# Optimization experiments

Hardware: AMD Instinct MI355X
Metric: run time of the kernel (lower is better)

## Reference

```python
import jax, jax.numpy as jnp
import numpy as np

B, C, H, W = 16, 64, 256, 256
STRIDE = 2
IN_KS = 3
OUT_KS = 3  # must be odd
HP, WP = H // STRIDE, W // STRIDE


def setup_inputs() -> dict:
    key = jax.random.key(0)
    k1, k2, k3 = jax.random.split(key, 3)
    f = jax.random.normal(k1, (B, C, HP, WP), dtype=jnp.float32)
    # Provenance: for pooled cell (i, j), the argmax location within the
    # IN_KS x IN_KS window anchored at (i*STRIDE, j*STRIDE), as a flat h*w index.
    dy = jax.random.randint(k2, (B, C, HP, WP), 0, IN_KS)
    dx = jax.random.randint(k3, (B, C, HP, WP), 0, IN_KS)
    rows = jnp.clip(jnp.arange(HP)[None, None, :, None] * STRIDE + dy, 0, H - 1)
    cols = jnp.clip(jnp.arange(WP)[None, None, None, :] * STRIDE + dx, 0, W - 1)
    provenance = (rows * W + cols).astype(jnp.int32)
    return {"f": f, "provenance": provenance, "h": H, "w": W}


def reference(f, provenance, h, w):
    b, c, hp, wp = f.shape
    # --- unpool: scatter pooled values to provenance locations in an h*w canvas ---
    vals = f.reshape(b * c, hp * wp)
    idx = provenance.reshape(b * c, hp * wp)
    scatter = lambda i, v: jnp.zeros((h * w,), f.dtype).at[i].set(v)
    up = jax.vmap(scatter)(idx, vals).reshape(b, c, h, w)
    # --- dilation: OUT_KS x OUT_KS windowed max, stride 1, 'same' padding ---
    p = (OUT_KS - 1) // 2
    out = jax.lax.reduce_window(
        up, -jnp.inf, jax.lax.max,
        window_dimensions=(1, 1, OUT_KS, OUT_KS),
        window_strides=(1, 1, 1, 1),
        padding=[(0, 0), (0, 0), (p, p), (p, p)],
    )
    return out
```

## Files before the change

### kernel.cpp

```cpp
#include <hip/hip_runtime.h>
#include <math.h>

#define BATCH 16
#define CHAN  64
#define Hh    256
#define Ww    256
#define HP    128
#define WP    128
#define TH    32
#define TW    32
#define CH    (TH + 2)
#define CW    (TW + 2)
#define CSU   35

typedef unsigned long long u64;

__global__ __launch_bounds__(256) void unpool_dilate_kernel(
    const float* __restrict__ f, const int* __restrict__ prov,
    float* __restrict__ out)
{
    __shared__ u64 s_cell[CH * CSU];

    const int tid = threadIdx.x;
    const int bc  = blockIdx.y;
    const int ty  = blockIdx.x >> 3;
    const int tx  = blockIdx.x & 7;
    const int y0  = ty * TH;
    const int x0  = tx * TW;

    const bool interior = (y0 != 0) & (y0 != Hh - TH) & (x0 != 0) & (x0 != Ww - TW);
    if (interior) {
        #pragma unroll
        for (int it = 0; it < 5; ++it) {
            const int idx = tid + it * 256;
            if (idx < CH * CSU) s_cell[idx] = 0ULL;
        }
    } else {
        #pragma unroll
        for (int it = 0; it < 5; ++it) {
            const int idx = tid + it * 256;
            if (idx < CH * CSU) {
                const int lr = idx / CSU;
                const int lc = idx - lr * CSU;
                const int r  = y0 - 1 + lr;
                const int c  = x0 - 1 + lc;
                const bool in = ((unsigned)r < Hh) & ((unsigned)c < Ww);
                s_cell[idx] = in ? 0ULL : 0xFF800000ULL;
            }
        }
    }

    const int pi_min = (y0 == 0) ? 0 : (y0 / 2 - 1);
    const int pj_min = (x0 == 0) ? 0 : (x0 / 2 - 1);
    const int pi_max = min(HP - 1, y0 / 2 + 16);
    const int pj_max = min(WP - 1, x0 / 2 + 16);
    const size_t in_base = (size_t)bc * (HP * WP);

    __syncthreads();

    #pragma unroll
    for (int it = 0; it < 2; ++it) {
        const int k = tid + it * 256;
        if (k < 18 * 18) {
            const int ki = k / 18;
            const int kj = k - ki * 18;
            const int pi = pi_min + ki;
            const int pj = pj_min + kj;
            if (pi <= pi_max && pj <= pj_max) {
                const int q = pi * WP + pj;
                const int p = prov[in_base + q];
                const int lr = (p >> 8) - y0 + 1;
                const int lc = (p & 255) - x0 + 1;
                if ((unsigned)lr < CH && (unsigned)lc < CW) {
                    const float fv = f[in_base + q];
                    const u64 v = ((u64)(unsigned)(q + 1) << 32) | __float_as_uint(fv);
                    atomicMax(&s_cell[lr * CSU + lc], v);
                }
            }
        }
    }
    __syncthreads();

    const int orow = tid >> 3;
    const int oc0  = (tid & 7) * 4;
    float vm[6];
    #pragma unroll
    for (int j = 0; j < 6; ++j) vm[j] = -INFINITY;
    #pragma unroll
    for (int dr = 0; dr < 3; ++dr) {
        const u64* row = &s_cell[(orow + dr) * CSU + oc0];
        #pragma unroll
        for (int j = 0; j < 6; ++j)
            vm[j] = fmaxf(vm[j], __uint_as_float((unsigned)row[j]));
    }
    float4 res;
    res.x = fmaxf(fmaxf(vm[0], vm[1]), vm[2]);
    res.y = fmaxf(fmaxf(vm[1], vm[2]), vm[3]);
    res.z = fmaxf(fmaxf(vm[2], vm[3]), vm[4]);
    res.w = fmaxf(fmaxf(vm[3], vm[4]), vm[5]);

    const size_t obase = (size_t)bc * (Hh * Ww)
                       + (size_t)(y0 + orow) * Ww + (x0 + oc0);
    *(float4*)(out + obase) = res;
}

extern "C" void kernel_launch(void* const* d_in, const int* in_sizes, int n_in,
                              void* d_out, int out_size, void* d_ws, size_t ws_size,
                              hipStream_t stream) {
    const float* f    = (const float*)d_in[0];
    const int*   prov = (const int*)d_in[1];
    float* out = (float*)d_out;

    dim3 grid((Hh / TH) * (Ww / TW), BATCH * CHAN);
    unpool_dilate_kernel<<<grid, 256, 0, stream>>>(f, prov, out);
}
```

Baseline: 436.5 us.

## Enlarge tiles to 64x64, use 32-bit key atomics and 4x4 register-blocked max

Doubles the tile to 64x64 so that halo and pooled-input overhead per output shrinks. It replaces the 64-bit packed atomicMax with a 32-bit atomicMax on the source index, followed by a resolve pass in which the winning thread writes its float value. Each thread now computes a 4x4 output block, reusing horizontal row maxima across rows to cut shared-memory reads. In exchange it adds an extra barrier and pass, and the -inf border writes are not ordered against other waves' zero-fill stores, which could race.

```diff
diff --git a/kernel.cpp b/kernel.cpp
--- a/kernel.cpp
+++ b/kernel.cpp
@@ -7,63 +7,60 @@
 #define Ww    256
 #define HP    128
 #define WP    128
-#define TH    32
-#define TW    32
-#define CH    (TH + 2)
-#define CW    (TW + 2)
-#define CSU   35
+#define TH    64
+#define TW    64
+#define CH    66
+#define CW    66
+#define CS    68
 
-typedef unsigned long long u64;
+typedef unsigned int u32;
 
-__global__ __launch_bounds__(256) void unpool_dilate_kernel(
+__global__ __launch_bounds__(256, 8) void unpool_dilate_kernel(
     const float* __restrict__ f, const int* __restrict__ prov,
     float* __restrict__ out)
 {
-    __shared__ u64 s_cell[CH * CSU];
+    __shared__ __align__(16) u32 s[CH * CS];
 
     const int tid = threadIdx.x;
     const int bc  = blockIdx.y;
-    const int ty  = blockIdx.x >> 3;
-    const int tx  = blockIdx.x & 7;
+    const int ty  = blockIdx.x >> 2;
+    const int tx  = blockIdx.x & 3;
     const int y0  = ty * TH;
     const int x0  = tx * TW;
 
-    const bool interior = (y0 != 0) & (y0 != Hh - TH) & (x0 != 0) & (x0 != Ww - TW);
-    if (interior) {
+    {
+        uint4* p4 = (uint4*)s;
+        const uint4 z = make_uint4(0u, 0u, 0u, 0u);
         #pragma unroll
         for (int it = 0; it < 5; ++it) {
             const int idx = tid + it * 256;
-            if (idx < CH * CSU) s_cell[idx] = 0ULL;
-        }
-    } else {
-        #pragma unroll
-        for (int it = 0; it < 5; ++it) {
-            const int idx = tid + it * 256;
-            if (idx < CH * CSU) {
-                const int lr = idx / CSU;
-                const int lc = idx - lr * CSU;
-                const int r  = y0 - 1 + lr;
-                const int c  = x0 - 1 + lc;
-                const bool in = ((unsigned)r < Hh) & ((unsigned)c < Ww);
-                s_cell[idx] = in ? 0ULL : 0xFF800000ULL;
-            }
+            if (idx < (CH * CS) / 4) p4[idx] = z;
         }
     }
+    const u32 NEGINF = 0xFF800000u;
+    if (ty == 0 && tid < CW) s[tid] = NEGINF;
+    if (ty == 3 && tid < CW) s[(CH - 1) * CS + tid] = NEGINF;
+    if (tx == 0 && tid < CH) s[tid * CS] = NEGINF;
+    if (tx == 3 && tid < CH) s[tid * CS + (CW - 1)] = NEGINF;
 
-    const int pi_min = (y0 == 0) ? 0 : (y0 / 2 - 1);
-    const int pj_min = (x0 == 0) ? 0 : (x0 / 2 - 1);
-    const int pi_max = min(HP - 1, y0 / 2 + 16);
-    const int pj_max = min(WP - 1, x0 / 2 + 16);
+    const int pi_min = (ty == 0) ? 0 : (ty * 32 - 1);
+    const int pj_min = (tx == 0) ? 0 : (tx * 32 - 1);
+    const int pi_max = min(HP - 1, ty * 32 + 32);
+    const int pj_max = min(WP - 1, tx * 32 + 32);
     const size_t in_base = (size_t)bc * (HP * WP);
 
     __syncthreads();
 
+    int   m_li[5];
+    u32   m_key[5];
+    float m_f[5];
     #pragma unroll
-    for (int it = 0; it < 2; ++it) {
+    for (int it = 0; it < 5; ++it) {
+        m_li[it] = -1;
         const int k = tid + it * 256;
-        if (k < 18 * 18) {
-            const int ki = k / 18;
-            const int kj = k - ki * 18;
+        if (k < 34 * 34) {
+            const int ki = k / 34;
+            const int kj = k - ki * 34;
             const int pi = pi_min + ki;
             const int pj = pj_min + kj;
             if (pi <= pi_max && pj <= pj_max) {
@@ -72,36 +69,54 @@
                 const int lr = (p >> 8) - y0 + 1;
                 const int lc = (p & 255) - x0 + 1;
                 if ((unsigned)lr < CH && (unsigned)lc < CW) {
-                    const float fv = f[in_base + q];
-                    const u64 v = ((u64)(unsigned)(q + 1) << 32) | __float_as_uint(fv);
-                    atomicMax(&s_cell[lr * CSU + lc], v);
+                    const int li = lr * CS + lc;
+                    m_li[it]  = li;
+                    m_key[it] = (u32)(q + 1);
+                    m_f[it]   = f[in_base + q];
+                    atomicMax(&s[li], (u32)(q + 1));
                 }
             }
         }
     }
     __syncthreads();
 
-    const int orow = tid >> 3;
-    const int oc0  = (tid & 7) * 4;
-    float vm[6];
     #pragma unroll
-    for (int j = 0; j < 6; ++j) vm[j] = -INFINITY;
+    for (int it = 0; it < 5; ++it) {
+        if (m_li[it] >= 0 && s[m_li[it]] == m_key[it])
+            s[m_li[it]] = __float_as_uint(m_f[it]);
+    }
+    __syncthreads();
+
+    const float* sf = (const float*)s;
+    const int tr = tid >> 4;
+    const int tc = tid & 15;
+    const int r0 = 4 * tr;
+    const int c0 = 4 * tc;
+
+    float h0[4], h1[4], h2[4];
+    const size_t obase = (size_t)bc * (Hh * Ww) + (size_t)(y0 + r0) * Ww + (x0 + c0);
+
     #pragma unroll
-    for (int dr = 0; dr < 3; ++dr) {
-        const u64* row = &s_cell[(orow + dr) * CSU + oc0];
+    for (int r = 0; r < 6; ++r) {
+        const float* row = sf + (r0 + r) * CS + c0;
+        const float4 a = *(const float4*)row;
+        const float2 b = *(const float2*)(row + 4);
+        float h[4];
+        h[0] = fmaxf(fmaxf(a.x, a.y), a.z);
+        h[1] = fmaxf(fmaxf(a.y, a.z), a.w);
+        h[2] = fmaxf(fmaxf(a.z, a.w), b.x);
+        h[3] = fmaxf(fmaxf(a.w, b.x), b.y);
+        if (r >= 2) {
+            float4 res;
+            res.x = fmaxf(fmaxf(h0[0], h1[0]), h[0]);
+            res.y = fmaxf(fmaxf(h0[1], h1[1]), h[1]);
+            res.z = fmaxf(fmaxf(h0[2], h1[2]), h[2]);
+            res.w = fmaxf(fmaxf(h0[3], h1[3]), h[3]);
+            *(float4*)(out + obase + (size_t)(r - 2) * Ww) = res;
+        }
         #pragma unroll
-        for (int j = 0; j < 6; ++j)
-            vm[j] = fmaxf(vm[j], __uint_as_float((unsigned)row[j]));
+        for (int j = 0; j < 4; ++j) { h0[j] = h1[j]; h1[j] = h[j]; }
     }
-    float4 res;
-    res.x = fmaxf(fmaxf(vm[0], vm[1]), vm[2]);
-    res.y = fmaxf(fmaxf(vm[1], vm[2]), vm[3]);
-    res.z = fmaxf(fmaxf(vm[2], vm[3]), vm[4]);
-    res.w = fmaxf(fmaxf(vm[3], vm[4]), vm[5]);
-
-    const size_t obase = (size_t)bc * (Hh * Ww)
-                       + (size_t)(y0 + orow) * Ww + (x0 + oc0);
-    *(float4*)(out + obase) = res;
 }
 
 extern "C" void kernel_launch(void* const* d_in, const int* in_sizes, int n_in,
```

Result: faster. 376.7 us (-13.7%).

## Replace shared-memory atomic scatter with register gather over 4x4 output patches

Applied to the files above, without the earlier changes.

Drops the shared-memory canvas built with 64-bit atomicMax and replaces it with a gather. Each block stages a 34x34 patch of (provenance, value) pairs in shared memory. Each thread then rebuilds a 6x6 window of the unpooled canvas in registers by comparing relative provenance offsets, and computes a 4x4 output patch. Tiles grow from 32x32 to 64x64, output uses nontemporal vector stores, and launch bounds request 4 blocks per CU. The goal is to remove atomic contention, the canvas initialization pass and extra synchronisation, at the cost of more register pressure and compare/select work per thread.

```diff
diff --git a/kernel.cpp b/kernel.cpp
--- a/kernel.cpp
+++ b/kernel.cpp
@@ -7,101 +7,114 @@
 #define Ww    256
 #define HP    128
 #define WP    128
-#define TH    32
-#define TW    32
-#define CH    (TH + 2)
-#define CW    (TW + 2)
-#define CSU   35
+#define TH    64
+#define TW    64
+#define PR    34
 
-typedef unsigned long long u64;
+typedef float vfloat4 __attribute__((ext_vector_type(4)));
 
-__global__ __launch_bounds__(256) void unpool_dilate_kernel(
+__global__ __launch_bounds__(256, 4) void unpool_dilate_kernel(
     const float* __restrict__ f, const int* __restrict__ prov,
     float* __restrict__ out)
 {
-    __shared__ u64 s_cell[CH * CSU];
+    __shared__ __align__(16) int2 sp[PR * PR];
 
     const int tid = threadIdx.x;
     const int bc  = blockIdx.y;
-    const int ty  = blockIdx.x >> 3;
-    const int tx  = blockIdx.x & 7;
+    const int ty  = blockIdx.x >> 2;
+    const int tx  = blockIdx.x & 3;
     const int y0  = ty * TH;
     const int x0  = tx * TW;
+    const int pi_base = (y0 >> 1) - 1;
+    const int pj_base = (x0 >> 1) - 1;
+    const size_t in_base = (size_t)bc * (HP * WP);
 
-    const bool interior = (y0 != 0) & (y0 != Hh - TH) & (x0 != 0) & (x0 != Ww - TW);
-    if (interior) {
+    #pragma unroll
+    for (int it = 0; it < 5; ++it) {
+        const int k = tid + it * 256;
+        if (k < PR * PR) {
+            const int li = k / PR;
+            const int lj = k - li * PR;
+            const int i  = min(max(pi_base + li, 0), HP - 1);
+            const int j  = min(max(pj_base + lj, 0), WP - 1);
+            const size_t g = in_base + (size_t)(i * WP + j);
+            sp[k] = make_int2(prov[g], __float_as_int(f[g]));
+        }
+    }
+    __syncthreads();
+
+    const int tr = tid >> 4;
+    const int tc = tid & 15;
+    const int r0 = y0 + 4 * tr;
+    const int c0 = x0 + 4 * tc;
+    const int base_rel = (r0 - 1) * 256 + (c0 - 1);
+
+    int   pr_[4][4];
+    float fv[4][4];
+    #pragma unroll
+    for (int d = 0; d < 4; ++d) {
+        const int rb = (2 * tr + d) * PR + 2 * tc;
+        const int4 pA = *(const int4*)&sp[rb];
+        const int4 pB = *(const int4*)&sp[rb + 2];
+        pr_[d][0] = pA.x - base_rel; fv[d][0] = __int_as_float(pA.y);
+        pr_[d][1] = pA.z - base_rel; fv[d][1] = __int_as_float(pA.w);
+        pr_[d][2] = pB.x - base_rel; fv[d][2] = __int_as_float(pB.y);
+        pr_[d][3] = pB.z - base_rel; fv[d][3] = __int_as_float(pB.w);
+    }
+
+    float val[6][6];
+    #pragma unroll
+    for (int a = 0; a < 6; ++a)
         #pragma unroll
-        for (int it = 0; it < 5; ++it) {
-            const int idx = tid + it * 256;
-            if (idx < CH * CSU) s_cell[idx] = 0ULL;
-        }
-    } else {
+        for (int b = 0; b < 6; ++b) val[a][b] = 0.0f;
+
+    constexpr int ALO[4] = {0, 1, 3, 5};
+    constexpr int AHI[4] = {1, 3, 5, 5};
+    #pragma unroll
+    for (int d = 0; d < 4; ++d) {
         #pragma unroll
-        for (int it = 0; it < 5; ++it) {
-            const int idx = tid + it * 256;
-            if (idx < CH * CSU) {
-                const int lr = idx / CSU;
-                const int lc = idx - lr * CSU;
-                const int r  = y0 - 1 + lr;
-                const int c  = x0 - 1 + lc;
-                const bool in = ((unsigned)r < Hh) & ((unsigned)c < Ww);
-                s_cell[idx] = in ? 0ULL : 0xFF800000ULL;
+        for (int e = 0; e < 4; ++e) {
+            const int   prel = pr_[d][e];
+            const float fc   = fv[d][e];
+            #pragma unroll
+            for (int a = ALO[d]; a <= AHI[d]; ++a) {
+                #pragma unroll
+                for (int b = ALO[e]; b <= AHI[e]; ++b) {
+                    val[a][b] = (prel == a * 256 + b) ? fc : val[a][b];
+                }
             }
         }
     }
 
-    const int pi_min = (y0 == 0) ? 0 : (y0 / 2 - 1);
-    const int pj_min = (x0 == 0) ? 0 : (x0 / 2 - 1);
-    const int pi_max = min(HP - 1, y0 / 2 + 16);
-    const int pj_max = min(WP - 1, x0 / 2 + 16);
-    const size_t in_base = (size_t)bc * (HP * WP);
-
-    __syncthreads();
-
-    #pragma unroll
-    for (int it = 0; it < 2; ++it) {
-        const int k = tid + it * 256;
-        if (k < 18 * 18) {
-            const int ki = k / 18;
-            const int kj = k - ki * 18;
-            const int pi = pi_min + ki;
-            const int pj = pj_min + kj;
-            if (pi <= pi_max && pj <= pj_max) {
-                const int q = pi * WP + pj;
-                const int p = prov[in_base + q];
-                const int lr = (p >> 8) - y0 + 1;
-                const int lc = (p & 255) - x0 + 1;
-                if ((unsigned)lr < CH && (unsigned)lc < CW) {
-                    const float fv = f[in_base + q];
-                    const u64 v = ((u64)(unsigned)(q + 1) << 32) | __float_as_uint(fv);
-                    atomicMax(&s_cell[lr * CSU + lc], v);
-                }
-            }
+    {
+        const bool e0 = (r0 == 0), e5 = (r0 == Hh - 4);
+        const bool g0 = (c0 == 0), g5 = (c0 == Ww - 4);
+        #pragma unroll
+        for (int b = 0; b < 6; ++b) {
+            val[0][b] = e0 ? -INFINITY : val[0][b];
+            val[5][b] = e5 ? -INFINITY : val[5][b];
+        }
+        #pragma unroll
+        for (int a = 0; a < 6; ++a) {
+            val[a][0] = g0 ? -INFINITY : val[a][0];
+            val[a][5] = g5 ? -INFINITY : val[a][5];
         }
     }
-    __syncthreads();
 
-    const int orow = tid >> 3;
-    const int oc0  = (tid & 7) * 4;
-    float vm[6];
+    const size_t obase = (size_t)bc * (Hh * Ww) + (size_t)r0 * Ww + c0;
     #pragma unroll
-    for (int j = 0; j < 6; ++j) vm[j] = -INFINITY;
-    #pragma unroll
-    for (int dr = 0; dr < 3; ++dr) {
-        const u64* row = &s_cell[(orow + dr) * CSU + oc0];
+    for (int p = 0; p < 4; ++p) {
+        float m[6];
         #pragma unroll
-        for (int j = 0; j < 6; ++j)
-            vm[j] = fmaxf(vm[j], __uint_as_float((unsigned)row[j]));
+        for (int b = 0; b < 6; ++b)
+            m[b] = fmaxf(fmaxf(val[p][b], val[p + 1][b]), val[p + 2][b]);
+        vfloat4 res;
+        res.x = fmaxf(fmaxf(m[0], m[1]), m[2]);
+        res.y = fmaxf(fmaxf(m[1], m[2]), m[3]);
+        res.z = fmaxf(fmaxf(m[2], m[3]), m[4]);
+        res.w = fmaxf(fmaxf(m[3], m[4]), m[5]);
+        __builtin_nontemporal_store(res, (vfloat4*)(out + obase + (size_t)p * Ww));
     }
-    float4 res;
-    res.x = fmaxf(fmaxf(vm[0], vm[1]), vm[2]);
-    res.y = fmaxf(fmaxf(vm[1], vm[2]), vm[3]);
-    res.z = fmaxf(fmaxf(vm[2], vm[3]), vm[4]);
-    res.w = fmaxf(fmaxf(vm[3], vm[4]), vm[5]);
-
-    const size_t obase = (size_t)bc * (Hh * Ww)
-                       + (size_t)(y0 + orow) * Ww + (x0 + oc0);
-    *(float4*)(out + obase) = res;
 }
 
 extern "C" void kernel_launch(void* const* d_in, const int* in_sizes, int n_in,
```

New measurement: 375.7 us. 1.16x faster.
